# Performance work log

Measured on AMD Instinct MI355X. Metric: run time of the kernel, lower is better.

The kernel has to match this reference:

```python
import jax, jax.numpy as jnp
import numpy as np

D_MODEL, D_STATE, D_CONV, EXPAND, DT_RANK = 1024, 16, 4, 2, 64
D_INNER = EXPAND * D_MODEL


def setup_inputs() -> dict:
    key = jax.random.key(0)
    ks = jax.random.split(key, 10)
    B, L = 2, 2048
    x = jax.random.normal(ks[0], (B, L, D_MODEL), dtype=jnp.float32)
    # torch nn.Linear weights are [out, in]; applied as x @ W.T
    in_proj_w = jax.random.normal(ks[1], (2 * D_INNER, D_MODEL), jnp.float32) * (D_MODEL ** -0.5)
    conv_w = jax.random.normal(ks[2], (D_INNER, 1, D_CONV), jnp.float32) * (D_CONV ** -0.5)
    conv_b = jax.random.normal(ks[3], (D_INNER,), jnp.float32) * 0.01
    x_proj_w = jax.random.normal(ks[4], (DT_RANK + 2 * D_STATE, D_INNER), jnp.float32) * (D_INNER ** -0.5)
    dt_init_std = DT_RANK ** -0.5
    dt_proj_w = jax.random.uniform(ks[5], (D_INNER, DT_RANK), jnp.float32, -dt_init_std, dt_init_std)
    # dt bias init: inverse-softplus of dt ~ LogUniform(1e-3, 1e-1)
    dt = jnp.exp(jax.random.uniform(ks[6], (D_INNER,), jnp.float32) * (np.log(0.1) - np.log(0.001)) + np.log(0.001))
    dt_proj_b = dt + jnp.log(-jnp.expm1(-dt))
    A_log = jnp.log(jnp.tile(jnp.arange(1, D_STATE + 1, dtype=jnp.float32), (D_INNER, 1)))  # [D_INNER, N]
    D_skip = jnp.ones((D_INNER,), jnp.float32)
    out_proj_w = jax.random.normal(ks[7], (D_MODEL, D_INNER), jnp.float32) * (D_INNER ** -0.5)
    return {"x": x, "in_proj_w": in_proj_w, "conv_w": conv_w, "conv_b": conv_b,
            "x_proj_w": x_proj_w, "dt_proj_w": dt_proj_w, "dt_proj_b": dt_proj_b,
            "A_log": A_log, "D_skip": D_skip, "out_proj_w": out_proj_w}


def selective_scan(u, delta, A, Bmat, Cmat, D_skip):
    # u, delta: [B, L, D]; A: [D, N]; Bmat, Cmat: [B, L, N]; D_skip: [D]
    def step(h, inp):
        delta_t, B_t, C_t, u_t = inp  # [B,D], [B,N], [B,N], [B,D]
        dA = jnp.exp(delta_t[..., None] * A)                      # [B,D,N]
        h = dA * h + (delta_t * u_t)[..., None] * B_t[:, None, :]  # [B,D,N]
        y_t = jnp.einsum('bdn,bn->bd', h, C_t)
        return h, y_t
    B_size, L, D_size = u.shape
    h0 = jnp.zeros((B_size, D_size, A.shape[-1]), u.dtype)
    xs = (jnp.swapaxes(delta, 0, 1), jnp.swapaxes(Bmat, 0, 1),
          jnp.swapaxes(Cmat, 0, 1), jnp.swapaxes(u, 0, 1))
    _, ys = jax.lax.scan(step, h0, xs)          # ys: [L, B, D]
    y = jnp.swapaxes(ys, 0, 1)                  # [B, L, D]
    return y + u * D_skip


def reference(x, in_proj_w, conv_w, conv_b, x_proj_w, dt_proj_w, dt_proj_b, A_log, D_skip, out_proj_w):
    B_size, L, _ = x.shape
    xz = x @ in_proj_w.T                         # [B, L, 2*D_INNER]
    x_ssm, z = jnp.split(xz, 2, axis=-1)
    # causal depthwise conv1d (torch pads d_conv-1 both sides then takes [:L])
    x_c = jnp.swapaxes(x_ssm, 1, 2)              # [B, D_INNER, L]
    x_c = jax.lax.conv_general_dilated(
        x_c, conv_w, window_strides=(1,), padding=[(D_CONV - 1, 0)],
        dimension_numbers=('NCH', 'OIH', 'NCH'), feature_group_count=D_INNER)
    x_c = x_c + conv_b[None, :, None]
    x_ssm = jax.nn.silu(jnp.swapaxes(x_c, 1, 2))  # [B, L, D_INNER]
    x_dbl = x_ssm @ x_proj_w.T                    # [B, L, dt_rank + 2N]
    dt, Bm, Cm = jnp.split(x_dbl, [DT_RANK, DT_RANK + D_STATE], axis=-1)
    delta = jax.nn.softplus(dt @ dt_proj_w.T + dt_proj_b)  # [B, L, D_INNER]
    A = -jnp.exp(A_log)                           # [D_INNER, N]
    y = selective_scan(x_ssm, delta, A, Bm, Cm, D_skip)
    y = y * jax.nn.silu(z)
    return y @ out_proj_w.T                       # [B, L, d_model]
```

## Files before the change

kernel.cpp:

```cpp
#include <hip/hip_runtime.h>
#include <hip/hip_bf16.h>
#include <math.h>

#define NB      2
#define LSEQ    2048
#define BLTOK   4096
#define DM      1024
#define DI      2048
#define NST     16
#define DTR     64
#define CH      128
#define LC      16
#define LOG2E   1.44269504f

typedef __attribute__((ext_vector_type(8))) short short8;
typedef __attribute__((ext_vector_type(4))) float f32x4;

#define LDS_PTR(p) ((__attribute__((address_space(3))) void*)(p))
#define GLB_PTR(p) ((const __attribute__((address_space(1))) void*)(p))

static __device__ __forceinline__ unsigned short f2bf(float f) {
    unsigned int u = __float_as_uint(f);
    unsigned int r = (u + 0x7FFFu + ((u >> 16) & 1u)) >> 16;
    return (unsigned short)r;
}
static __device__ __forceinline__ float bf2f(unsigned short v) {
    return __uint_as_float((unsigned int)v << 16);
}

static __device__ __forceinline__ void pow_tree(float w, float* e) {
    e[0]  = w;
    e[1]  = e[0] * e[0];
    e[2]  = e[1] * e[0];
    e[3]  = e[1] * e[1];
    e[4]  = e[3] * e[0];
    e[5]  = e[3] * e[1];
    e[6]  = e[3] * e[2];
    e[7]  = e[3] * e[3];
    e[8]  = e[7] * e[0];
    e[9]  = e[7] * e[1];
    e[10] = e[7] * e[2];
    e[11] = e[7] * e[3];
    e[12] = e[7] * e[4];
    e[13] = e[7] * e[5];
    e[14] = e[7] * e[6];
    e[15] = e[7] * e[7];
}

__launch_bounds__(256)
__global__ void cast_bf16(const float* __restrict__ in, unsigned short* __restrict__ out, int n4)
{
    int i = blockIdx.x * 256 + threadIdx.x;
    if (i < n4) {
        float4 v = ((const float4*)in)[i];
        uint2 o;
        o.x = (unsigned)f2bf(v.x) | ((unsigned)f2bf(v.y) << 16);
        o.y = (unsigned)f2bf(v.z) | ((unsigned)f2bf(v.w) << 16);
        ((uint2*)out)[i] = o;
    }
}

template<int EPI>
__launch_bounds__(256)
__global__ void gemm_db(const unsigned short* __restrict__ A,
                        const unsigned short* __restrict__ W,
                        void* __restrict__ Cout,
                        const float* __restrict__ bias,
                        int M, int N, int K, int lda, int ldb, int ldc)
{
    __shared__ unsigned short lds[2][2][128 * 64];

    const int tid = threadIdx.x;
    const int l = tid & 63;
    const int w = tid >> 6;
    const int wr = w >> 1, wc = w & 1;
    const int brow = blockIdx.y * 128;
    const int bcol = blockIdx.x * 128;

    const int strow = tid >> 3;
    const int scol  = ((tid & 7) ^ (strow & 7)) * 8;

    f32x4 acc[4][4];
#pragma unroll
    for (int i = 0; i < 4; ++i)
#pragma unroll
        for (int j = 0; j < 4; ++j) acc[i][j] = (f32x4)0.f;

    auto stage = [&](int bb, int k0) {
#pragma unroll
        for (int i = 0; i < 4; ++i) {
            const unsigned short* ga = A + (size_t)(brow + i * 32 + strow) * lda + k0 + scol;
            __builtin_amdgcn_global_load_lds(GLB_PTR(ga),
                LDS_PTR((char*)&lds[bb][0][0] + (i * 32 + w * 8) * 128), 16, 0, 0);
            const unsigned short* gb = W + (size_t)(bcol + i * 32 + strow) * ldb + k0 + scol;
            __builtin_amdgcn_global_load_lds(GLB_PTR(gb),
                LDS_PTR((char*)&lds[bb][1][0] + (i * 32 + w * 8) * 128), 16, 0, 0);
        }
    };

    auto compute = [&](int bb) {
        const char* baseA = (const char*)&lds[bb][0][0];
        const char* baseB = (const char*)&lds[bb][1][0];
        const int xo  = (l & 7) * 16;
        const int ko0 = (l >> 4) * 16;
#pragma unroll
        for (int ks = 0; ks < 2; ++ks) {
            const int kb = ks * 64 + ko0;
            short8 af[4], bfr[4];
#pragma unroll
            for (int i = 0; i < 4; ++i) {
                const int rowA = wr * 64 + i * 16 + (l & 15);
                af[i] = *(const short8*)(baseA + rowA * 128 + (kb ^ xo));
                const int rowB = wc * 64 + i * 16 + (l & 15);
                bfr[i] = *(const short8*)(baseB + rowB * 128 + (kb ^ xo));
            }
#pragma unroll
            for (int i = 0; i < 4; ++i)
#pragma unroll
                for (int j = 0; j < 4; ++j)
                    acc[i][j] = __builtin_amdgcn_mfma_f32_16x16x32_bf16(af[i], bfr[j], acc[i][j], 0, 0, 0);
        }
    };

    const int nt = K / 64;
    stage(0, 0);
    __syncthreads();
    int cur = 0;
    for (int t = 0; t < nt - 1; ++t) {
        stage(cur ^ 1, (t + 1) * 64);
        compute(cur);
        __syncthreads();
        cur ^= 1;
    }
    compute(cur);

#pragma unroll
    for (int i = 0; i < 4; ++i) {
        const int row0 = brow + wr * 64 + i * 16 + ((l >> 4) * 4);
#pragma unroll
        for (int j = 0; j < 4; ++j) {
            const int col = bcol + wc * 64 + j * 16 + (l & 15);
            if (EPI == 1) {
                unsigned short* Cb = (unsigned short*)Cout;
#pragma unroll
                for (int r = 0; r < 4; ++r)
                    Cb[(size_t)(row0 + r) * ldc + col] = f2bf(acc[i][j][r]);
            } else if (EPI == 2) {
                float* Cf = (float*)Cout;
                const float bv = bias[col];
#pragma unroll
                for (int r = 0; r < 4; ++r) {
                    float v = acc[i][j][r] + bv;
                    Cf[(size_t)(row0 + r) * ldc + col] = (v > 20.f) ? v : log1pf(__expf(v));
                }
            } else {
                float* Cf = (float*)Cout;
#pragma unroll
                for (int r = 0; r < 4; ++r)
                    Cf[(size_t)(row0 + r) * ldc + col] = acc[i][j][r];
            }
        }
    }
}

__launch_bounds__(256)
__global__ void gemm_mfma_sk(const unsigned short* __restrict__ A,
                             const unsigned short* __restrict__ W,
                             float* __restrict__ Cpart,
                             int M, int N, int K, int lda, int ldb, int ldc, int kslices)
{
    __shared__ unsigned short Asub[128 * 32];
    __shared__ unsigned short Bsub[128 * 32];

    const int tid = threadIdx.x;
    const int l = tid & 63;
    const int w = tid >> 6;
    const int wr = w >> 1, wc = w & 1;
    const int brow = blockIdx.y * 128;
    const int bcol = blockIdx.x * 128;
    const int ks = blockIdx.z;
    const int klen = K / kslices;
    const int kbeg = ks * klen;
    float* C = Cpart + (size_t)ks * M * ldc;

    f32x4 acc[4][4];
#pragma unroll
    for (int i = 0; i < 4; ++i)
#pragma unroll
        for (int j = 0; j < 4; ++j) acc[i][j] = (f32x4)0.f;

    const int srow = tid >> 2;
    const int scol = (tid & 3) * 8;

    for (int k0 = kbeg; k0 < kbeg + klen; k0 += 32) {
#pragma unroll
        for (int i = 0; i < 2; ++i) {
            const int ar = brow + i * 64 + srow;
            const unsigned short* ga = A + (size_t)ar * lda + k0 + scol;
            __builtin_amdgcn_global_load_lds(GLB_PTR(ga),
                LDS_PTR((char*)Asub + i * 4096 + w * 1024), 16, 0, 0);
            int nr = bcol + i * 64 + srow;
            if (nr > N - 1) nr = N - 1;
            const unsigned short* gb = W + (size_t)nr * ldb + k0 + scol;
            __builtin_amdgcn_global_load_lds(GLB_PTR(gb),
                LDS_PTR((char*)Bsub + i * 4096 + w * 1024), 16, 0, 0);
        }
        __syncthreads();

        short8 af[4], bf[4];
#pragma unroll
        for (int i = 0; i < 4; ++i) {
            const int row = wr * 64 + i * 16 + (l & 15);
            af[i] = *(const short8*)((const char*)Asub + row * 64 + (l >> 4) * 16);
        }
#pragma unroll
        for (int j = 0; j < 4; ++j) {
            const int row = wc * 64 + j * 16 + (l & 15);
            bf[j] = *(const short8*)((const char*)Bsub + row * 64 + (l >> 4) * 16);
        }
#pragma unroll
        for (int i = 0; i < 4; ++i)
#pragma unroll
            for (int j = 0; j < 4; ++j)
                acc[i][j] = __builtin_amdgcn_mfma_f32_16x16x32_bf16(af[i], bf[j], acc[i][j], 0, 0, 0);
        __syncthreads();
    }

#pragma unroll
    for (int i = 0; i < 4; ++i) {
        const int row0 = brow + wr * 64 + i * 16 + ((l >> 4) * 4);
#pragma unroll
        for (int j = 0; j < 4; ++j) {
            const int col = bcol + wc * 64 + j * 16 + (l & 15);
            if (col < N) {
#pragma unroll
                for (int r = 0; r < 4; ++r)
                    C[(size_t)(row0 + r) * ldc + col] = acc[i][j][r];
            }
        }
    }
}

__launch_bounds__(256)
__global__ void sk_reduce(const float* __restrict__ part, float* __restrict__ out,
                          unsigned short* __restrict__ dtb, int n4, int slices)
{
    int i = blockIdx.x * 256 + threadIdx.x;
    if (i < n4) {
        float4 s = ((const float4*)part)[i];
        for (int k = 1; k < slices; ++k) {
            float4 p = ((const float4*)part)[(size_t)k * n4 + i];
            s.x += p.x; s.y += p.y; s.z += p.z; s.w += p.w;
        }
        ((float4*)out)[i] = s;
        const int r = i / 24, cq = i % 24;
        if (cq < 16) {
            uint2 o;
            o.x = (unsigned)f2bf(s.x) | ((unsigned)f2bf(s.y) << 16);
            o.y = (unsigned)f2bf(s.z) | ((unsigned)f2bf(s.w) << 16);
            *(uint2*)&dtb[(size_t)r * DTR + cq * 4] = o;
        }
    }
}

__launch_bounds__(256)
__global__ void conv_silu_kernel(const unsigned short* __restrict__ xzb,
                                 const float* __restrict__ cw,
                                 const float* __restrict__ cb,
                                 unsigned short* __restrict__ ub)
{
    const int orig = blockIdx.x;
    const int bl = (orig & 7) * (BLTOK / 8) + (orig >> 3);
    const int l  = bl & (LSEQ - 1);
    const int d0 = threadIdx.x * 8;

    float acc[8];
    float4 w4[8];
#pragma unroll
    for (int q = 0; q < 8; ++q) {
        w4[q]  = *(const float4*)&cw[(d0 + q) * 4];
        acc[q] = cb[d0 + q];
    }
#pragma unroll
    for (int k = 0; k < 4; ++k) {
        const int ls = l - 3 + k;
        if (ls < 0) continue;
        short8 v = *(const short8*)&xzb[(size_t)(bl - 3 + k) * (2 * DI) + d0];
#pragma unroll
        for (int q = 0; q < 8; ++q) {
            const float wk = ((const float*)&w4[q])[k];
            acc[q] = fmaf(wk, bf2f((unsigned short)v[q]), acc[q]);
        }
    }
    short8 o;
#pragma unroll
    for (int q = 0; q < 8; ++q) {
        const float s = acc[q] / (1.f + __expf(-acc[q]));
        o[q] = (short)f2bf(s);
    }
    *(short8*)&ub[(size_t)bl * DI + d0] = o;
}

__launch_bounds__(256)
__global__ void scan_phase1(const float* __restrict__ delta, const unsigned short* __restrict__ ub,
                            const float* __restrict__ xdbl, const float* __restrict__ A_log,
                            float* __restrict__ P, float* __restrict__ S)
{
    __shared__ float sB[LC][NST];
    const int tid = threadIdx.x;
    const int d = blockIdx.x * 256 + tid;
    const int c = blockIdx.y;
    const int b = blockIdx.z;
    const int t0 = c * LC;

    for (int i = tid; i < LC * NST; i += 256)
        sB[i >> 4][i & 15] = xdbl[(size_t)(b * LSEQ + t0 + (i >> 4)) * 96 + 64 + (i & 15)];
    __syncthreads();

    const float Av0 = -__expf(A_log[d * NST]) * LOG2E;
    bool fast = true;
    for (int n = 1; n < NST; ++n) {
        const float avn = -__expf(A_log[d * NST + n]) * LOG2E;
        fast &= (fabsf(avn - (float)(n + 1) * Av0) <= 1e-3f * fabsf(avn));
    }

    float Sv[NST];
    float dsum = 0.f;
#pragma unroll
    for (int n = 0; n < NST; ++n) Sv[n] = 0.f;

    const float*          dbase = delta + (size_t)(b * LSEQ + t0) * DI + d;
    const unsigned short* ubase = ub    + (size_t)(b * LSEQ + t0) * DI + d;

    if (fast) {
        for (int tg = 0; tg < LC; tg += 4) {
            float dl[4], uu[4];
#pragma unroll
            for (int q = 0; q < 4; ++q) {
                dl[q] = dbase[(size_t)(tg + q) * DI];
                uu[q] = bf2f(ubase[(size_t)(tg + q) * DI]);
            }
#pragma unroll
            for (int q = 0; q < 4; ++q) {
                const float du = dl[q] * uu[q];
                dsum += dl[q];
                float e[NST];
                pow_tree(__builtin_amdgcn_exp2f(dl[q] * Av0), e);
#pragma unroll
                for (int n = 0; n < NST; ++n)
                    Sv[n] = fmaf(e[n], Sv[n], du * sB[tg + q][n]);
            }
        }
        float Pv[NST];
        pow_tree(__builtin_amdgcn_exp2f(dsum * Av0), Pv);
        const size_t base = ((size_t)(b * CH + c) * DI + d) * NST;
#pragma unroll
        for (int n = 0; n < NST; n += 4) {
            *(f32x4*)&P[base + n] = (f32x4){Pv[n], Pv[n+1], Pv[n+2], Pv[n+3]};
            *(f32x4*)&S[base + n] = (f32x4){Sv[n], Sv[n+1], Sv[n+2], Sv[n+3]};
        }
    } else {
        for (int t = 0; t < LC; ++t) {
            const float dlt = dbase[(size_t)t * DI];
            const float uu  = bf2f(ubase[(size_t)t * DI]);
            const float du  = dlt * uu;
            dsum += dlt;
            for (int n = 0; n < NST; ++n) {
                const float avn = -__expf(A_log[d * NST + n]) * LOG2E;
                const float dA = __builtin_amdgcn_exp2f(dlt * avn);
                Sv[n] = fmaf(dA, Sv[n], du * sB[t][n]);
            }
        }
        const size_t base = ((size_t)(b * CH + c) * DI + d) * NST;
        for (int n = 0; n < NST; ++n) {
            const float avn = -__expf(A_log[d * NST + n]) * LOG2E;
            P[base + n] = __builtin_amdgcn_exp2f(dsum * avn);
            S[base + n] = Sv[n];
        }
    }
}

__launch_bounds__(256)
__global__ void scan_phase2(const float* __restrict__ P, const float* __restrict__ S,
                            float* __restrict__ hin)
{
    const int g = blockIdx.x * 256 + threadIdx.x;
    const int n = g & 15;
    const int d = (g >> 4) & (DI - 1);
    const int b = g >> 15;
    float h = 0.f;
#pragma unroll 4
    for (int c = 0; c < CH; ++c) {
        const size_t idx = ((size_t)(b * CH + c) * DI + d) * NST + n;
        hin[idx] = h;
        h = fmaf(P[idx], h, S[idx]);
    }
}

__launch_bounds__(256)
__global__ void scan_phase3(const float* __restrict__ delta, const unsigned short* __restrict__ ub,
                            const float* __restrict__ xdbl, const float* __restrict__ A_log,
                            const float* __restrict__ Dskip, const unsigned short* __restrict__ xzb,
                            const float* __restrict__ hin, unsigned short* __restrict__ yg)
{
    __shared__ float sB[LC][NST], sC[LC][NST];
    const int tid = threadIdx.x;
    const int d = blockIdx.x * 256 + tid;
    const int c = blockIdx.y;
    const int b = blockIdx.z;
    const int t0 = c * LC;

    for (int i = tid; i < LC * NST; i += 256) {
        const size_t row = (size_t)(b * LSEQ + t0 + (i >> 4)) * 96;
        sB[i >> 4][i & 15] = xdbl[row + 64 + (i & 15)];
        sC[i >> 4][i & 15] = xdbl[row + 80 + (i & 15)];
    }
    __syncthreads();

    const float Av0 = -__expf(A_log[d * NST]) * LOG2E;
    bool fast = true;
    for (int n = 1; n < NST; ++n) {
        const float avn = -__expf(A_log[d * NST + n]) * LOG2E;
        fast &= (fabsf(avn - (float)(n + 1) * Av0) <= 1e-3f * fabsf(avn));
    }

    float h[NST];
    const size_t hbase = ((size_t)(b * CH + c) * DI + d) * NST;
#pragma unroll
    for (int n = 0; n < NST; n += 4) {
        f32x4 t = *(const f32x4*)&hin[hbase + n];
        h[n] = t.x; h[n+1] = t.y; h[n+2] = t.z; h[n+3] = t.w;
    }
    const float Dskv = Dskip[d];

    const float*          dbase = delta + (size_t)(b * LSEQ + t0) * DI + d;
    const unsigned short* ubase = ub    + (size_t)(b * LSEQ + t0) * DI + d;
    const unsigned short* zbase = xzb   + (size_t)(b * LSEQ + t0) * (2 * DI) + DI + d;
    unsigned short* yrow = yg + (size_t)(b * LSEQ + t0) * DI + d;

    if (fast) {
        for (int tg = 0; tg < LC; tg += 4) {
            float dl[4], uu[4], zz[4];
#pragma unroll
            for (int q = 0; q < 4; ++q) {
                dl[q] = dbase[(size_t)(tg + q) * DI];
                uu[q] = bf2f(ubase[(size_t)(tg + q) * DI]);
                zz[q] = bf2f(zbase[(size_t)(tg + q) * (2 * DI)]);
            }
#pragma unroll
            for (int q = 0; q < 4; ++q) {
                const float du = dl[q] * uu[q];
                float e[NST];
                pow_tree(__builtin_amdgcn_exp2f(dl[q] * Av0), e);
                float y = 0.f;
#pragma unroll
                for (int n = 0; n < NST; ++n) {
                    h[n] = fmaf(e[n], h[n], du * sB[tg + q][n]);
                    y = fmaf(h[n], sC[tg + q][n], y);
                }
                const float zv = zz[q];
                const float sig = __frcp_rn(1.f + __expf(-zv));
                const float val = (y + uu[q] * Dskv) * (zv * sig);
                yrow[(size_t)(tg + q) * DI] = f2bf(val);
            }
        }
    } else {
        for (int t = 0; t < LC; ++t) {
            const float dlt = dbase[(size_t)t * DI];
            const float uu  = bf2f(ubase[(size_t)t * DI]);
            const float zv  = bf2f(zbase[(size_t)t * (2 * DI)]);
            const float du  = dlt * uu;
            float y = 0.f;
            for (int n = 0; n < NST; ++n) {
                const float avn = -__expf(A_log[d * NST + n]) * LOG2E;
                const float dA = __builtin_amdgcn_exp2f(dlt * avn);
                h[n] = fmaf(dA, h[n], du * sB[t][n]);
                y = fmaf(h[n], sC[t][n], y);
            }
            const float sig = __frcp_rn(1.f + __expf(-zv));
            const float val = (y + uu * Dskv) * (zv * sig);
            yrow[(size_t)t * DI] = f2bf(val);
        }
    }
}

extern "C" void kernel_launch(void* const* d_in, const int* in_sizes, int n_in,
                              void* d_out, int out_size, void* d_ws, size_t ws_size,
                              hipStream_t stream)
{
    const float* x        = (const float*)d_in[0];
    const float* in_w     = (const float*)d_in[1];
    const float* conv_w   = (const float*)d_in[2];
    const float* conv_b   = (const float*)d_in[3];
    const float* xproj_w  = (const float*)d_in[4];
    const float* dtproj_w = (const float*)d_in[5];
    const float* dtproj_b = (const float*)d_in[6];
    const float* A_log    = (const float*)d_in[7];
    const float* Dskip    = (const float*)d_in[8];
    const float* out_w    = (const float*)d_in[9];
    float* out = (float*)d_out;

    char* ws = (char*)d_ws;
#define MB(x) ((size_t)(x) * 1024 * 1024)
    unsigned short* xzb   = (unsigned short*)(ws);
    unsigned short* ub    = (unsigned short*)(ws + MB(32));
    float*          delta = (float*)(ws + MB(48));
    float*          xdbl  = (float*)(ws + MB(80));
    unsigned short* ygb   = (unsigned short*)(ws + MB(82));
    float*          P     = (float*)(ws + MB(98));
    float*          S     = (float*)(ws + MB(130));
    float*          hin   = (float*)(ws + MB(162));
    unsigned short* xb    = (unsigned short*)(ws + MB(194));
    unsigned short* wb1   = (unsigned short*)(ws + MB(202));
    unsigned short* wb3   = (unsigned short*)(ws + MB(210));
    unsigned short* wb6   = (unsigned short*)(ws + MB(211));
    unsigned short* wb5   = (unsigned short*)(ws + MB(215));
    unsigned short* dtb   = (unsigned short*)(ws + MB(216));
    float*          xdbl_part = P;

    dim3 blk(256);

    cast_bf16<<<dim3((BLTOK * DM / 4 + 255) / 256), blk, 0, stream>>>(x, xb, BLTOK * DM / 4);
    cast_bf16<<<dim3((2 * DI * DM / 4 + 255) / 256), blk, 0, stream>>>(in_w, wb1, 2 * DI * DM / 4);
    cast_bf16<<<dim3((96 * DI / 4 + 255) / 256), blk, 0, stream>>>(xproj_w, wb3, 96 * DI / 4);
    cast_bf16<<<dim3((DM * DI / 4 + 255) / 256), blk, 0, stream>>>(out_w, wb6, DM * DI / 4);
    cast_bf16<<<dim3((DI * DTR / 4 + 255) / 256), blk, 0, stream>>>(dtproj_w, wb5, DI * DTR / 4);

    gemm_db<1><<<dim3(32, 32), blk, 0, stream>>>(xb, wb1, xzb, nullptr,
                                                 BLTOK, 2 * DI, DM, DM, DM, 2 * DI);

    conv_silu_kernel<<<dim3(BLTOK), blk, 0, stream>>>(xzb, conv_w, conv_b, ub);

    gemm_mfma_sk<<<dim3(1, 32, 8), blk, 0, stream>>>(ub, wb3, xdbl_part,
                                                     BLTOK, DTR + 2 * NST, DI, DI, DI, 96, 8);
    sk_reduce<<<dim3((BLTOK * 96 / 4 + 255) / 256), blk, 0, stream>>>(xdbl_part, xdbl, dtb,
                                                                      BLTOK * 96 / 4, 8);

    gemm_db<2><<<dim3(16, 32), blk, 0, stream>>>(dtb, wb5, delta, dtproj_b,
                                                 BLTOK, DI, DTR, DTR, DTR, DI);

    scan_phase1<<<dim3(DI / 256, CH, NB), blk, 0, stream>>>(delta, ub, xdbl, A_log, P, S);
    scan_phase2<<<dim3(NB * DI * NST / 256), blk, 0, stream>>>(P, S, hin);
    scan_phase3<<<dim3(DI / 256, CH, NB), blk, 0, stream>>>(delta, ub, xdbl, A_log, Dskip,
                                                            xzb, hin, ygb);

    gemm_db<0><<<dim3(8, 32), blk, 0, stream>>>(ygb, wb6, out, nullptr,
                                                BLTOK, DM, DI, DI, DI, DM);
}
```

Baseline: 254.6 us.

## Store delta in bf16, drop P buffer, merge casts, halve scan chunk count

The five cast kernels become one launch. The delta GEMM epilogue now writes softplus output as bf16 instead of fp32, which halves delta traffic into both scan phases. Phase 1 no longer writes the per-chunk decay P; it writes only a scalar dsum per channel, and phase 2 recomputes the decay with exp2 from dsum and A_log. The chunk count drops from 128 to 64 with chunk length 32, which shrinks the S and hin buffers but halves parallelism in phases 1 and 3; delta in bf16 also costs accuracy.

```diff
diff --git a/kernel.cpp b/kernel.cpp
--- a/kernel.cpp
+++ b/kernel.cpp
@@ -9,8 +9,8 @@
 #define DI      2048
 #define NST     16
 #define DTR     64
-#define CH      128
-#define LC      16
+#define CH      64
+#define LC      32
 #define LOG2E   1.44269504f
 
 typedef __attribute__((ext_vector_type(8))) short short8;
@@ -47,17 +47,33 @@
     e[15] = e[7] * e[7];
 }
 
-__launch_bounds__(256)
-__global__ void cast_bf16(const float* __restrict__ in, unsigned short* __restrict__ out, int n4)
+#define C4_X   (BLTOK * DM / 4)
+#define C4_W1  (2 * DI * DM / 4)
+#define C4_W3  (96 * DI / 4)
+#define C4_W6  (DM * DI / 4)
+#define C4_W5  (DI * DTR / 4)
+#define C4_TOT (C4_X + C4_W1 + C4_W3 + C4_W6 + C4_W5)
+
+__launch_bounds__(256)
+__global__ void cast_all(const float* __restrict__ x,   unsigned short* __restrict__ xb,
+                         const float* __restrict__ w1,  unsigned short* __restrict__ wb1,
+                         const float* __restrict__ w3,  unsigned short* __restrict__ wb3,
+                         const float* __restrict__ w6,  unsigned short* __restrict__ wb6,
+                         const float* __restrict__ w5,  unsigned short* __restrict__ wb5)
 {
     int i = blockIdx.x * 256 + threadIdx.x;
-    if (i < n4) {
-        float4 v = ((const float4*)in)[i];
-        uint2 o;
-        o.x = (unsigned)f2bf(v.x) | ((unsigned)f2bf(v.y) << 16);
-        o.y = (unsigned)f2bf(v.z) | ((unsigned)f2bf(v.w) << 16);
-        ((uint2*)out)[i] = o;
-    }
+    if (i >= C4_TOT) return;
+    const float* in; unsigned short* out;
+    if (i < C4_X)                         { in = x;  out = xb;  }
+    else if ((i -= C4_X) < C4_W1)         { in = w1; out = wb1; }
+    else if ((i -= C4_W1) < C4_W3)        { in = w3; out = wb3; }
+    else if ((i -= C4_W3) < C4_W6)        { in = w6; out = wb6; }
+    else       { i -= C4_W6;                in = w5; out = wb5; }
+    float4 v = ((const float4*)in)[i];
+    uint2 o;
+    o.x = (unsigned)f2bf(v.x) | ((unsigned)f2bf(v.y) << 16);
+    o.y = (unsigned)f2bf(v.z) | ((unsigned)f2bf(v.w) << 16);
+    ((uint2*)out)[i] = o;
 }
 
 template<int EPI>
@@ -145,13 +161,14 @@
 #pragma unroll
                 for (int r = 0; r < 4; ++r)
                     Cb[(size_t)(row0 + r) * ldc + col] = f2bf(acc[i][j][r]);
-            } else if (EPI == 2) {
-                float* Cf = (float*)Cout;
+            } else if (EPI == 2 || EPI == 3) {
                 const float bv = bias[col];
 #pragma unroll
                 for (int r = 0; r < 4; ++r) {
                     float v = acc[i][j][r] + bv;
-                    Cf[(size_t)(row0 + r) * ldc + col] = (v > 20.f) ? v : log1pf(__expf(v));
+                    v = (v > 20.f) ? v : log1pf(__expf(v));
+                    if (EPI == 2) ((float*)Cout)[(size_t)(row0 + r) * ldc + col] = v;
+                    else ((unsigned short*)Cout)[(size_t)(row0 + r) * ldc + col] = f2bf(v);
                 }
             } else {
                 float* Cf = (float*)Cout;
@@ -302,9 +319,10 @@
 }
 
 __launch_bounds__(256)
-__global__ void scan_phase1(const float* __restrict__ delta, const unsigned short* __restrict__ ub,
+__global__ void scan_phase1(const unsigned short* __restrict__ delta,
+                            const unsigned short* __restrict__ ub,
                             const float* __restrict__ xdbl, const float* __restrict__ A_log,
-                            float* __restrict__ P, float* __restrict__ S)
+                            float* __restrict__ S, float* __restrict__ dsum_out)
 {
     __shared__ float sB[LC][NST];
     const int tid = threadIdx.x;
@@ -329,7 +347,7 @@
 #pragma unroll
     for (int n = 0; n < NST; ++n) Sv[n] = 0.f;
 
-    const float*          dbase = delta + (size_t)(b * LSEQ + t0) * DI + d;
+    const unsigned short* dbase = delta + (size_t)(b * LSEQ + t0) * DI + d;
     const unsigned short* ubase = ub    + (size_t)(b * LSEQ + t0) * DI + d;
 
     if (fast) {
@@ -337,7 +355,7 @@
             float dl[4], uu[4];
 #pragma unroll
             for (int q = 0; q < 4; ++q) {
-                dl[q] = dbase[(size_t)(tg + q) * DI];
+                dl[q] = bf2f(dbase[(size_t)(tg + q) * DI]);
                 uu[q] = bf2f(ubase[(size_t)(tg + q) * DI]);
             }
 #pragma unroll
@@ -351,17 +369,9 @@
                     Sv[n] = fmaf(e[n], Sv[n], du * sB[tg + q][n]);
             }
         }
-        float Pv[NST];
-        pow_tree(__builtin_amdgcn_exp2f(dsum * Av0), Pv);
-        const size_t base = ((size_t)(b * CH + c) * DI + d) * NST;
-#pragma unroll
-        for (int n = 0; n < NST; n += 4) {
-            *(f32x4*)&P[base + n] = (f32x4){Pv[n], Pv[n+1], Pv[n+2], Pv[n+3]};
-            *(f32x4*)&S[base + n] = (f32x4){Sv[n], Sv[n+1], Sv[n+2], Sv[n+3]};
-        }
     } else {
         for (int t = 0; t < LC; ++t) {
-            const float dlt = dbase[(size_t)t * DI];
+            const float dlt = bf2f(dbase[(size_t)t * DI]);
             const float uu  = bf2f(ubase[(size_t)t * DI]);
             const float du  = dlt * uu;
             dsum += dlt;
@@ -371,34 +381,36 @@
                 Sv[n] = fmaf(dA, Sv[n], du * sB[t][n]);
             }
         }
-        const size_t base = ((size_t)(b * CH + c) * DI + d) * NST;
-        for (int n = 0; n < NST; ++n) {
-            const float avn = -__expf(A_log[d * NST + n]) * LOG2E;
-            P[base + n] = __builtin_amdgcn_exp2f(dsum * avn);
-            S[base + n] = Sv[n];
-        }
-    }
-}
-
-__launch_bounds__(256)
-__global__ void scan_phase2(const float* __restrict__ P, const float* __restrict__ S,
-                            float* __restrict__ hin)
+    }
+
+    const size_t base = ((size_t)(b * CH + c) * DI + d) * NST;
+#pragma unroll
+    for (int n = 0; n < NST; n += 4)
+        *(f32x4*)&S[base + n] = (f32x4){Sv[n], Sv[n+1], Sv[n+2], Sv[n+3]};
+    dsum_out[(size_t)(b * CH + c) * DI + d] = dsum;
+}
+
+__launch_bounds__(256)
+__global__ void scan_phase2(const float* __restrict__ S, const float* __restrict__ dsum,
+                            const float* __restrict__ A_log, float* __restrict__ hin)
 {
     const int g = blockIdx.x * 256 + threadIdx.x;
     const int n = g & 15;
     const int d = (g >> 4) & (DI - 1);
     const int b = g >> 15;
+    const float avn = -__expf(A_log[d * NST + n]) * LOG2E;
     float h = 0.f;
-#pragma unroll 4
     for (int c = 0; c < CH; ++c) {
         const size_t idx = ((size_t)(b * CH + c) * DI + d) * NST + n;
         hin[idx] = h;
-        h = fmaf(P[idx], h, S[idx]);
-    }
-}
-
-__launch_bounds__(256)
-__global__ void scan_phase3(const float* __restrict__ delta, const unsigned short* __restrict__ ub,
+        const float Pc = __builtin_amdgcn_exp2f(dsum[(size_t)(b * CH + c) * DI + d] * avn);
+        h = fmaf(Pc, h, S[idx]);
+    }
+}
+
+__launch_bounds__(256)
+__global__ void scan_phase3(const unsigned short* __restrict__ delta,
+                            const unsigned short* __restrict__ ub,
                             const float* __restrict__ xdbl, const float* __restrict__ A_log,
                             const float* __restrict__ Dskip, const unsigned short* __restrict__ xzb,
                             const float* __restrict__ hin, unsigned short* __restrict__ yg)
@@ -433,7 +445,7 @@
     }
     const float Dskv = Dskip[d];
 
-    const float*          dbase = delta + (size_t)(b * LSEQ + t0) * DI + d;
+    const unsigned short* dbase = delta + (size_t)(b * LSEQ + t0) * DI + d;
     const unsigned short* ubase = ub    + (size_t)(b * LSEQ + t0) * DI + d;
     const unsigned short* zbase = xzb   + (size_t)(b * LSEQ + t0) * (2 * DI) + DI + d;
     unsigned short* yrow = yg + (size_t)(b * LSEQ + t0) * DI + d;
@@ -443,7 +455,7 @@
             float dl[4], uu[4], zz[4];
 #pragma unroll
             for (int q = 0; q < 4; ++q) {
-                dl[q] = dbase[(size_t)(tg + q) * DI];
+                dl[q] = bf2f(dbase[(size_t)(tg + q) * DI]);
                 uu[q] = bf2f(ubase[(size_t)(tg + q) * DI]);
                 zz[q] = bf2f(zbase[(size_t)(tg + q) * (2 * DI)]);
             }
@@ -466,7 +478,7 @@
         }
     } else {
         for (int t = 0; t < LC; ++t) {
-            const float dlt = dbase[(size_t)t * DI];
+            const float dlt = bf2f(dbase[(size_t)t * DI]);
             const float uu  = bf2f(ubase[(size_t)t * DI]);
             const float zv  = bf2f(zbase[(size_t)t * (2 * DI)]);
             const float du  = dlt * uu;
@@ -504,27 +516,24 @@
 #define MB(x) ((size_t)(x) * 1024 * 1024)
     unsigned short* xzb   = (unsigned short*)(ws);
     unsigned short* ub    = (unsigned short*)(ws + MB(32));
-    float*          delta = (float*)(ws + MB(48));
-    float*          xdbl  = (float*)(ws + MB(80));
-    unsigned short* ygb   = (unsigned short*)(ws + MB(82));
-    float*          P     = (float*)(ws + MB(98));
-    float*          S     = (float*)(ws + MB(130));
-    float*          hin   = (float*)(ws + MB(162));
-    unsigned short* xb    = (unsigned short*)(ws + MB(194));
-    unsigned short* wb1   = (unsigned short*)(ws + MB(202));
-    unsigned short* wb3   = (unsigned short*)(ws + MB(210));
-    unsigned short* wb6   = (unsigned short*)(ws + MB(211));
-    unsigned short* wb5   = (unsigned short*)(ws + MB(215));
-    unsigned short* dtb   = (unsigned short*)(ws + MB(216));
-    float*          xdbl_part = P;
+    unsigned short* delta = (unsigned short*)(ws + MB(48));
+    float*          xdbl  = (float*)(ws + MB(64));
+    unsigned short* ygb   = (unsigned short*)(ws + MB(66));
+    float*          S     = (float*)(ws + MB(82));
+    float*          dsum  = (float*)(ws + MB(98));
+    float*          hin   = (float*)(ws + MB(99));
+    unsigned short* xb    = (unsigned short*)(ws + MB(115));
+    unsigned short* wb1   = (unsigned short*)(ws + MB(123));
+    unsigned short* wb3   = (unsigned short*)(ws + MB(131));
+    unsigned short* wb6   = (unsigned short*)(ws + MB(132));
+    unsigned short* wb5   = (unsigned short*)(ws + MB(136));
+    unsigned short* dtb   = (unsigned short*)(ws + MB(137));
+    float*          xdbl_part = S;
 
     dim3 blk(256);
 
-    cast_bf16<<<dim3((BLTOK * DM / 4 + 255) / 256), blk, 0, stream>>>(x, xb, BLTOK * DM / 4);
-    cast_bf16<<<dim3((2 * DI * DM / 4 + 255) / 256), blk, 0, stream>>>(in_w, wb1, 2 * DI * DM / 4);
-    cast_bf16<<<dim3((96 * DI / 4 + 255) / 256), blk, 0, stream>>>(xproj_w, wb3, 96 * DI / 4);
-    cast_bf16<<<dim3((DM * DI / 4 + 255) / 256), blk, 0, stream>>>(out_w, wb6, DM * DI / 4);
-    cast_bf16<<<dim3((DI * DTR / 4 + 255) / 256), blk, 0, stream>>>(dtproj_w, wb5, DI * DTR / 4);
+    cast_all<<<dim3((C4_TOT + 255) / 256), blk, 0, stream>>>(x, xb, in_w, wb1, xproj_w, wb3,
+                                                             out_w, wb6, dtproj_w, wb5);
 
     gemm_db<1><<<dim3(32, 32), blk, 0, stream>>>(xb, wb1, xzb, nullptr,
                                                  BLTOK, 2 * DI, DM, DM, DM, 2 * DI);
@@ -536,11 +545,11 @@
     sk_reduce<<<dim3((BLTOK * 96 / 4 + 255) / 256), blk, 0, stream>>>(xdbl_part, xdbl, dtb,
                                                                       BLTOK * 96 / 4, 8);
 
-    gemm_db<2><<<dim3(16, 32), blk, 0, stream>>>(dtb, wb5, delta, dtproj_b,
+    gemm_db<3><<<dim3(16, 32), blk, 0, stream>>>(dtb, wb5, delta, dtproj_b,
                                                  BLTOK, DI, DTR, DTR, DTR, DI);
 
-    scan_phase1<<<dim3(DI / 256, CH, NB), blk, 0, stream>>>(delta, ub, xdbl, A_log, P, S);
-    scan_phase2<<<dim3(NB * DI * NST / 256), blk, 0, stream>>>(P, S, hin);
+    scan_phase1<<<dim3(DI / 256, CH, NB), blk, 0, stream>>>(delta, ub, xdbl, A_log, S, dsum);
+    scan_phase2<<<dim3(NB * DI * NST / 256), blk, 0, stream>>>(S, dsum, A_log, hin);
     scan_phase3<<<dim3(DI / 256, CH, NB), blk, 0, stream>>>(delta, ub, xdbl, A_log, Dskip,
                                                             xzb, hin, ygb);
 
```

Measured after the change: 219.6 us. 13.8% less time.
